# Optimization experiments

Hardware: AMD Instinct MI355X
Metric: run time of the kernel (lower is better)

Reference implementation:

```python
import jax, jax.numpy as jnp
import numpy as np

B, S, D, H = 2, 2048, 1024, 16
DK = D // H  # 64
THETA = 10000.0


def setup_inputs() -> dict:
    key = jax.random.key(0)
    ks = jax.random.split(key, 5)
    sigma = (2.0 / (D + DK)) ** 0.5
    return {
        "x": jax.random.normal(ks[0], (B, S, D), jnp.float32),
        "Wq": jax.random.normal(ks[1], (D, H * DK), jnp.float32) * sigma,
        "Wk": jax.random.normal(ks[2], (D, H * DK), jnp.float32) * sigma,
        "Wv": jax.random.normal(ks[3], (D, H * DK), jnp.float32) * sigma,
        "Wo": jax.random.normal(ks[4], (D, H * DK), jnp.float32) * sigma,
        "token_positions": jnp.arange(S, dtype=jnp.int32),
    }


def _rope(x, pos):
    # x: (B, H, S, DK); pos: (S,). Block-diag 2x2 rotation == paired rotation.
    half = DK // 2
    k = jnp.arange(half, dtype=jnp.float32)
    inv_freq = 1.0 / (THETA ** (2.0 * k / DK))          # (half,)
    ang = pos.astype(jnp.float32)[:, None] * inv_freq    # (S, half)
    cos, sin = jnp.cos(ang), jnp.sin(ang)
    xr = x.reshape(*x.shape[:-1], half, 2)
    x0, x1 = xr[..., 0], xr[..., 1]
    o0 = x0 * cos - x1 * sin
    o1 = x0 * sin + x1 * cos
    return jnp.stack([o0, o1], axis=-1).reshape(x.shape)


def reference(x, Wq, Wk, Wv, Wo, token_positions):
    # projections: einsum('... d_in, hd d_in -> ... hd') == x @ W.T
    def proj(W):
        return (x @ W.T).reshape(B, S, H, DK).transpose(0, 2, 1, 3)  # (B,H,S,DK)

    q, k, v = proj(Wq), proj(Wk), proj(Wv)
    q = _rope(q, token_positions)
    k = _rope(k, token_positions)

    scores = jnp.einsum("bhqd,bhkd->bhqk", q, k) / jnp.sqrt(jnp.float32(DK))
    causal = jnp.tril(jnp.ones((S, S), bool))  # (S,S), True where attended
    scores = jnp.where(causal[None, None], scores, -jnp.inf)
    probs = jax.nn.softmax(scores, axis=-1)

    o = jnp.einsum("bhqk,bhkd->bhqd", probs, v)
    o = o.transpose(0, 2, 1, 3).reshape(B, S, H * DK)
    return o @ Wo.T  # einsum('... d_out, d_model d_out -> ... d_model')
```

## Files before the change

kernel.cpp:

```cpp
#include <hip/hip_runtime.h>

typedef __bf16 bf16;
typedef __bf16 bf16x4 __attribute__((ext_vector_type(4)));
typedef __bf16 bf16x8 __attribute__((ext_vector_type(8)));
typedef float f32x4 __attribute__((ext_vector_type(4)));

#define MFMA16(a, b, c) __builtin_amdgcn_mfma_f32_16x16x32_bf16((a), (b), (c), 0, 0, 0)

constexpr int B_ = 2, S_ = 2048, D_ = 1024, H_ = 16, DK_ = 64;

__device__ __forceinline__ void gload16(const bf16* g, bf16* l)
{
  __builtin_amdgcn_global_load_lds(
      (const __attribute__((address_space(1))) uint32_t*)g,
      (__attribute__((address_space(3))) uint32_t*)l, 16, 0, 0);
}

__global__ __launch_bounds__(256) void cvt_k(
    const float* __restrict__ x, const float* __restrict__ Wq, const float* __restrict__ Wk,
    const float* __restrict__ Wv, const float* __restrict__ Wo, bf16* __restrict__ ws)
{
  size_t f = ((size_t)blockIdx.x * 256 + threadIdx.x) * 4;
  const float* src;
  bf16* dst;
  size_t off;
  if (f < 4194304) {
    src = x; dst = ws; off = f;
  } else {
    size_t g = f - 4194304;
    int wsel = (int)(g >> 20);
    off = g & 1048575;
    src = wsel == 0 ? Wq : wsel == 1 ? Wk : wsel == 2 ? Wv : Wo;
    dst = ws + 4194304 + ((size_t)wsel << 20);
  }
  float4 v = *(const float4*)(src + off);
  bf16x4 o = {(bf16)v.x, (bf16)v.y, (bf16)v.z, (bf16)v.w};
  *(bf16x4*)(dst + off) = o;
}

template <typename TY, int PERM>
__global__ __launch_bounds__(256) void gemm_k(
    const bf16* __restrict__ A,
    const bf16* __restrict__ W0, const bf16* __restrict__ W1, const bf16* __restrict__ W2,
    TY* __restrict__ Y0, TY* __restrict__ Y1, TY* __restrict__ Y2,
    int Kdim, float scale0)
{
  __shared__ __align__(16) bf16 As[128 * 64];
  __shared__ __align__(16) bf16 Bs[128 * 64];
  const int t = threadIdx.x, l = t & 63, w = t >> 6;
  const int wm = w >> 1, wn = w & 1;
  const int m0 = blockIdx.x * 128, n0 = blockIdx.y * 128;
  const int z = blockIdx.z;
  const bf16* W = z == 0 ? W0 : z == 1 ? W1 : W2;
  TY* Y = z == 0 ? Y0 : z == 1 ? Y1 : Y2;
  const float scale = (PERM == 1 && z == 0) ? scale0 : 1.0f;

  f32x4 acc[4][4] = {};

  for (int k0 = 0; k0 < Kdim; k0 += 64) {
    __syncthreads();
#pragma unroll
    for (int j = 0; j < 4; ++j) {
      int slot = j * 256 + t;
      int row = slot >> 3, c8 = slot & 7;
      int csw = (c8 ^ (row & 7)) << 3;
      gload16(A + (size_t)(m0 + row) * Kdim + k0 + csw, &As[(j * 256 + w * 64) * 8]);
      gload16(W + (size_t)(n0 + row) * Kdim + k0 + csw, &Bs[(j * 256 + w * 64) * 8]);
    }
    asm volatile("s_waitcnt vmcnt(0)" ::: "memory");
    __syncthreads();
#pragma unroll
    for (int kk = 0; kk < 2; ++kk) {
      bf16x8 af[4], bfr[4];
#pragma unroll
      for (int i = 0; i < 4; ++i) {
        int Ra = wm * 64 + i * 16 + (l & 15);
        int Rb = wn * 64 + i * 16 + (l & 15);
        int c = kk * 4 + (l >> 4);
        af[i] = *(const bf16x8*)&As[Ra * 64 + ((c ^ (Ra & 7)) << 3)];
        bfr[i] = *(const bf16x8*)&Bs[Rb * 64 + ((c ^ (Rb & 7)) << 3)];
      }
#pragma unroll
      for (int mi = 0; mi < 4; ++mi)
#pragma unroll
        for (int ni = 0; ni < 4; ++ni)
          acc[mi][ni] = MFMA16(af[mi], bfr[ni], acc[mi][ni]);
    }
  }

#pragma unroll
  for (int mi = 0; mi < 4; ++mi)
#pragma unroll
    for (int ni = 0; ni < 4; ++ni)
#pragma unroll
      for (int j = 0; j < 4; ++j) {
        int m = m0 + wm * 64 + mi * 16 + (l >> 4) * 4 + j;
        int n = n0 + wn * 64 + ni * 16 + (l & 15);
        float v = acc[mi][ni][j] * scale;
        if (PERM == 0) {
          Y[(size_t)m * 1024 + n] = (TY)v;
        } else {
          int b = m >> 11, s = m & (S_ - 1), h = n >> 6, d = n & (DK_ - 1);
          Y[(((size_t)(b * H_ + h)) * S_ + s) * DK_ + d] = (TY)v;
        }
      }
}

__global__ __launch_bounds__(256) void rope_k(
    bf16* __restrict__ K, const int* __restrict__ pos)
{
  int idx = blockIdx.x * 256 + threadIdx.x;
  int kpg = idx & 3;
  int s = (idx >> 2) & (S_ - 1);
  int bh = idx >> 13;
  float p = (float)pos[s];
  size_t off = ((size_t)bh * S_ + s) * DK_ + kpg * 16;
  bf16x8 lo = *(const bf16x8*)(K + off);
  bf16x8 hi = *(const bf16x8*)(K + off + 8);
  bf16x8 olo, ohi;
#pragma unroll
  for (int ii = 0; ii < 8; ++ii) {
    int kp = kpg * 8 + ii;
    float ang = p * exp2f((float)kp * -0.41524101186017f);
    float sn, cs;
    __sincosf(ang, &sn, &cs);
    float x0 = (float)((ii < 4 ? lo : hi)[(ii & 3) * 2]);
    float x1 = (float)((ii < 4 ? lo : hi)[(ii & 3) * 2 + 1]);
    bf16 o0 = (bf16)(x0 * cs - x1 * sn);
    bf16 o1 = (bf16)(x0 * sn + x1 * cs);
    if (ii < 4) { olo[(ii & 3) * 2] = o0; olo[(ii & 3) * 2 + 1] = o1; }
    else        { ohi[(ii & 3) * 2] = o0; ohi[(ii & 3) * 2 + 1] = o1; }
  }
  *(bf16x8*)(K + off) = olo;
  *(bf16x8*)(K + off + 8) = ohi;
}

__global__ __launch_bounds__(256, 4) void attn_k(
    const bf16* __restrict__ Q, const bf16* __restrict__ K, const bf16* __restrict__ V,
    const int* __restrict__ pos, bf16* __restrict__ O)
{
  __shared__ __align__(16) bf16 Klds[2][64 * 64];
  __shared__ __align__(16) bf16 Vt[2][64 * 64];
  __shared__ __align__(16) bf16 Ps[4][16 * 64];

  const int t = threadIdx.x, l = t & 63, w = t >> 6;
  const int bx = blockIdx.x;
  const int i5 = bx >> 5;
  const int bh = bx & 31;
  const int a = i5 & 7, bq = i5 >> 3;
  const int qt = (bq == 0) ? (31 - a) : (bq == 1) ? a : (bq == 2) ? (16 + a) : (15 - a);
  const int b = bh >> 4, h = bh & 15;
  const size_t base = (size_t)bh * S_ * DK_;
  const int q0 = qt * 64;

  const int qrow = w * 16 + (l & 15), qcol = (l >> 4) * 8;
  const bf16* pq = Q + base + (size_t)(q0 + qrow) * 64 + qcol;
  bf16x8 aq0 = *(const bf16x8*)pq, aq1 = *(const bf16x8*)(pq + 32);
  {
    float p = (float)pos[q0 + qrow];
#pragma unroll
    for (int i2 = 0; i2 < 4; ++i2) {
      int kp = (l >> 4) * 4 + i2;
      float s0, c0, s1, c1;
      __sincosf(p * exp2f((float)kp * -0.41524101186017f), &s0, &c0);
      __sincosf(p * exp2f((float)(kp + 16) * -0.41524101186017f), &s1, &c1);
      float x0 = (float)aq0[2 * i2], x1 = (float)aq0[2 * i2 + 1];
      aq0[2 * i2] = (bf16)(x0 * c0 - x1 * s0);
      aq0[2 * i2 + 1] = (bf16)(x0 * s0 + x1 * c0);
      x0 = (float)aq1[2 * i2]; x1 = (float)aq1[2 * i2 + 1];
      aq1[2 * i2] = (bf16)(x0 * c1 - x1 * s1);
      aq1[2 * i2 + 1] = (bf16)(x0 * s1 + x1 * c1);
    }
  }

  {
#pragma unroll
    for (int j = 0; j < 2; ++j) {
      int slot = j * 256 + t, row = slot >> 3, c8 = slot & 7;
      gload16(K + base + (size_t)row * 64 + ((c8 ^ (row & 7)) << 3),
              &Klds[0][(j * 256 + w * 64) * 8]);
    }
    const bf16* pv = V + base + (size_t)l * 64 + w * 16;
    bf16x8 v0 = *(const bf16x8*)pv, v1 = *(const bf16x8*)(pv + 8);
    asm volatile("s_waitcnt vmcnt(0)" ::: "memory");
#pragma unroll
    for (int ii = 0; ii < 8; ++ii) {
      int d0 = w * 16 + ii, d1 = w * 16 + 8 + ii;
      Vt[0][d0 * 64 + (((l >> 3) ^ (d0 & 7)) << 3) + (l & 7)] = v0[ii];
      Vt[0][d1 * 64 + (((l >> 3) ^ (d1 & 7)) << 3) + (l & 7)] = v1[ii];
    }
  }
  __syncthreads();

  f32x4 acc[4] = {};
  float lsum[4] = {0.f, 0.f, 0.f, 0.f};

  int cur = 0;
  for (int tk = 0; tk <= qt; ++tk) {
    const int nxt = cur ^ 1;
    const bool hasn = tk < qt;
    bf16x8 v0, v1;
    if (hasn) {
      const int kv0n = (tk + 1) * 64;
#pragma unroll
      for (int j = 0; j < 2; ++j) {
        int slot = j * 256 + t, row = slot >> 3, c8 = slot & 7;
        gload16(K + base + (size_t)(kv0n + row) * 64 + ((c8 ^ (row & 7)) << 3),
                &Klds[nxt][(j * 256 + w * 64) * 8]);
      }
      const bf16* pv = V + base + (size_t)(kv0n + l) * 64 + w * 16;
      v0 = *(const bf16x8*)pv;
      v1 = *(const bf16x8*)(pv + 8);
    }

    f32x4 sc[4];
    __builtin_amdgcn_s_setprio(1);
#pragma unroll
    for (int nf = 0; nf < 4; ++nf) {
      int R = nf * 16 + (l & 15);
      int c0 = l >> 4;
      bf16x8 b0 = *(const bf16x8*)&Klds[cur][R * 64 + ((c0 ^ (R & 7)) << 3)];
      bf16x8 b1 = *(const bf16x8*)&Klds[cur][R * 64 + (((4 + c0) ^ (R & 7)) << 3)];
      f32x4 s = {};
      s = MFMA16(aq0, b0, s);
      s = MFMA16(aq1, b1, s);
      sc[nf] = s;
    }
    __builtin_amdgcn_s_setprio(0);

    if (tk == qt) {
#pragma unroll
      for (int nf = 0; nf < 4; ++nf)
#pragma unroll
        for (int j = 0; j < 4; ++j) {
          int kvl = nf * 16 + (l & 15);
          int ql = w * 16 + (l >> 4) * 4 + j;
          if (kvl > ql) sc[nf][j] = -1e30f;
        }
    }

#pragma unroll
    for (int nf = 0; nf < 4; ++nf)
#pragma unroll
      for (int j = 0; j < 4; ++j) {
        float p = exp2f(sc[nf][j]);
        lsum[j] += p;
        int r = (l >> 4) * 4 + j, c = nf * 16 + (l & 15);
        Ps[w][r * 64 + ((((c >> 3) ^ (r & 7))) << 3) + (c & 7)] = (bf16)p;
      }

    asm volatile("s_waitcnt lgkmcnt(0)" ::: "memory");

    __builtin_amdgcn_s_setprio(1);
#pragma unroll
    for (int kk = 0; kk < 2; ++kk) {
      int rp = l & 15;
      int c8p = kk * 4 + (l >> 4);
      bf16x8 ap = *(const bf16x8*)&Ps[w][rp * 64 + ((c8p ^ (rp & 7)) << 3)];
#pragma unroll
      for (int nf = 0; nf < 4; ++nf) {
        int R = nf * 16 + (l & 15);
        bf16x8 bv = *(const bf16x8*)&Vt[cur][R * 64 + ((c8p ^ (R & 7)) << 3)];
        acc[nf] = MFMA16(ap, bv, acc[nf]);
      }
    }
    __builtin_amdgcn_s_setprio(0);

    if (hasn) {
#pragma unroll
      for (int ii = 0; ii < 8; ++ii) {
        int d0 = w * 16 + ii, d1 = w * 16 + 8 + ii;
        Vt[nxt][d0 * 64 + (((l >> 3) ^ (d0 & 7)) << 3) + (l & 7)] = v0[ii];
        Vt[nxt][d1 * 64 + (((l >> 3) ^ (d1 & 7)) << 3) + (l & 7)] = v1[ii];
      }
      asm volatile("s_waitcnt vmcnt(0)" ::: "memory");
    }
    __syncthreads();
    cur = nxt;
  }

#pragma unroll
  for (int m = 1; m <= 8; m <<= 1)
#pragma unroll
    for (int j = 0; j < 4; ++j)
      lsum[j] += __shfl_xor(lsum[j], m, 64);

#pragma unroll
  for (int nf = 0; nf < 4; ++nf)
#pragma unroll
    for (int j = 0; j < 4; ++j) {
      int r = w * 16 + (l >> 4) * 4 + j;
      int d = nf * 16 + (l & 15);
      O[((size_t)(b * S_ + q0 + r) * H_ + h) * DK_ + d] = (bf16)(acc[nf][j] / lsum[j]);
    }
}

extern "C" void kernel_launch(void* const* d_in, const int* in_sizes, int n_in,
                              void* d_out, int out_size, void* d_ws, size_t ws_size,
                              hipStream_t stream)
{
  const float* x = (const float*)d_in[0];
  const float* Wq = (const float*)d_in[1];
  const float* Wk = (const float*)d_in[2];
  const float* Wv = (const float*)d_in[3];
  const float* Wo = (const float*)d_in[4];
  const int* pos = (const int*)d_in[5];

  bf16* ws = (bf16*)d_ws;
  const size_t NE = (size_t)B_ * H_ * S_ * DK_;
  bf16* xb = ws;
  bf16* Wqb = ws + NE;
  bf16* Wkb = Wqb + 1048576;
  bf16* Wvb = Wkb + 1048576;
  bf16* Wob = Wvb + 1048576;
  bf16* Qb = Wob + 1048576;
  bf16* Kb = Qb + NE;
  bf16* Vb = Kb + NE;
  bf16* Ob = xb;

  dim3 blk(256);

  hipLaunchKernelGGL(cvt_k, dim3(8192), blk, 0, stream, x, Wq, Wk, Wv, Wo, ws);

  hipLaunchKernelGGL((gemm_k<bf16, 1>), dim3(32, 8, 3), blk, 0, stream,
                     xb, Wqb, Wkb, Wvb, Qb, Kb, Vb, 1024, 0.125f * 1.4426950408889634f);

  hipLaunchKernelGGL(rope_k, dim3(1024), blk, 0, stream, Kb, pos);

  hipLaunchKernelGGL(attn_k, dim3(1024), blk, 0, stream, Qb, Kb, Vb, pos, Ob);

  hipLaunchKernelGGL((gemm_k<float, 0>), dim3(32, 8, 1), blk, 0, stream,
                     Ob, Wob, Wob, Wob, (float*)d_out, (float*)d_out, (float*)d_out,
                     1024, 1.0f);
}
```

Baseline: 128.5 us.

## Enlarge attention blocks to 128 query rows with 8 waves sharing KV tiles

The attention kernel now runs 512-thread blocks covering 128 query rows (two 64-row query tiles), so each K/V tile loaded into LDS is reused by twice as many waves. Loads per thread are halved, and waves whose query tile is already finished skip compute on the last KV tile. This cuts global K/V traffic and the number of blocks, but halves the grid to 512 blocks. It also adds idle waves on the diagonal tile and puts more waves behind each barrier.

```diff
diff --git a/kernel.cpp b/kernel.cpp
--- a/kernel.cpp
+++ b/kernel.cpp
@@ -135,23 +135,26 @@
   *(bf16x8*)(K + off + 8) = ohi;
 }
 
-__global__ __launch_bounds__(256, 4) void attn_k(
+__global__ __launch_bounds__(512, 2) void attn_k(
     const bf16* __restrict__ Q, const bf16* __restrict__ K, const bf16* __restrict__ V,
     const int* __restrict__ pos, bf16* __restrict__ O)
 {
   __shared__ __align__(16) bf16 Klds[2][64 * 64];
   __shared__ __align__(16) bf16 Vt[2][64 * 64];
-  __shared__ __align__(16) bf16 Ps[4][16 * 64];
+  __shared__ __align__(16) bf16 Ps[8][16 * 64];
 
   const int t = threadIdx.x, l = t & 63, w = t >> 6;
+  const int wl = w & 3;
   const int bx = blockIdx.x;
   const int i5 = bx >> 5;
   const int bh = bx & 31;
   const int a = i5 & 7, bq = i5 >> 3;
-  const int qt = (bq == 0) ? (31 - a) : (bq == 1) ? a : (bq == 2) ? (16 + a) : (15 - a);
+  const int qt2 = bq ? a : (15 - a);
   const int b = bh >> 4, h = bh & 15;
   const size_t base = (size_t)bh * S_ * DK_;
-  const int q0 = qt * 64;
+  const int q0 = qt2 * 128;
+  const int ntk = 2 * qt2 + 2;
+  const int myqt = 2 * qt2 + (w >> 2);
 
   const int qrow = w * 16 + (l & 15), qcol = (l >> 4) * 8;
   const bf16* pq = Q + base + (size_t)(q0 + qrow) * 64 + qcol;
@@ -174,20 +177,16 @@
   }
 
   {
-#pragma unroll
-    for (int j = 0; j < 2; ++j) {
-      int slot = j * 256 + t, row = slot >> 3, c8 = slot & 7;
-      gload16(K + base + (size_t)row * 64 + ((c8 ^ (row & 7)) << 3),
-              &Klds[0][(j * 256 + w * 64) * 8]);
-    }
-    const bf16* pv = V + base + (size_t)l * 64 + w * 16;
-    bf16x8 v0 = *(const bf16x8*)pv, v1 = *(const bf16x8*)(pv + 8);
+    int row = t >> 3, c8 = t & 7;
+    gload16(K + base + (size_t)row * 64 + ((c8 ^ (row & 7)) << 3),
+            &Klds[0][(w * 64) * 8]);
+    const bf16* pv = V + base + (size_t)l * 64 + w * 8;
+    bf16x8 v0 = *(const bf16x8*)pv;
     asm volatile("s_waitcnt vmcnt(0)" ::: "memory");
 #pragma unroll
     for (int ii = 0; ii < 8; ++ii) {
-      int d0 = w * 16 + ii, d1 = w * 16 + 8 + ii;
+      int d0 = w * 8 + ii;
       Vt[0][d0 * 64 + (((l >> 3) ^ (d0 & 7)) << 3) + (l & 7)] = v0[ii];
-      Vt[0][d1 * 64 + (((l >> 3) ^ (d1 & 7)) << 3) + (l & 7)] = v1[ii];
     }
   }
   __syncthreads();
@@ -196,82 +195,78 @@
   float lsum[4] = {0.f, 0.f, 0.f, 0.f};
 
   int cur = 0;
-  for (int tk = 0; tk <= qt; ++tk) {
+  for (int tk = 0; tk < ntk; ++tk) {
     const int nxt = cur ^ 1;
-    const bool hasn = tk < qt;
-    bf16x8 v0, v1;
+    const bool hasn = (tk + 1) < ntk;
+    bf16x8 v0;
     if (hasn) {
       const int kv0n = (tk + 1) * 64;
-#pragma unroll
-      for (int j = 0; j < 2; ++j) {
-        int slot = j * 256 + t, row = slot >> 3, c8 = slot & 7;
-        gload16(K + base + (size_t)(kv0n + row) * 64 + ((c8 ^ (row & 7)) << 3),
-                &Klds[nxt][(j * 256 + w * 64) * 8]);
-      }
-      const bf16* pv = V + base + (size_t)(kv0n + l) * 64 + w * 16;
-      v0 = *(const bf16x8*)pv;
-      v1 = *(const bf16x8*)(pv + 8);
-    }
-
-    f32x4 sc[4];
-    __builtin_amdgcn_s_setprio(1);
-#pragma unroll
-    for (int nf = 0; nf < 4; ++nf) {
-      int R = nf * 16 + (l & 15);
-      int c0 = l >> 4;
-      bf16x8 b0 = *(const bf16x8*)&Klds[cur][R * 64 + ((c0 ^ (R & 7)) << 3)];
-      bf16x8 b1 = *(const bf16x8*)&Klds[cur][R * 64 + (((4 + c0) ^ (R & 7)) << 3)];
-      f32x4 s = {};
-      s = MFMA16(aq0, b0, s);
-      s = MFMA16(aq1, b1, s);
-      sc[nf] = s;
-    }
-    __builtin_amdgcn_s_setprio(0);
-
-    if (tk == qt) {
-#pragma unroll
-      for (int nf = 0; nf < 4; ++nf)
-#pragma unroll
-        for (int j = 0; j < 4; ++j) {
-          int kvl = nf * 16 + (l & 15);
-          int ql = w * 16 + (l >> 4) * 4 + j;
-          if (kvl > ql) sc[nf][j] = -1e30f;
-        }
-    }
-
-#pragma unroll
-    for (int nf = 0; nf < 4; ++nf)
-#pragma unroll
-      for (int j = 0; j < 4; ++j) {
-        float p = exp2f(sc[nf][j]);
-        lsum[j] += p;
-        int r = (l >> 4) * 4 + j, c = nf * 16 + (l & 15);
-        Ps[w][r * 64 + ((((c >> 3) ^ (r & 7))) << 3) + (c & 7)] = (bf16)p;
-      }
-
-    asm volatile("s_waitcnt lgkmcnt(0)" ::: "memory");
-
-    __builtin_amdgcn_s_setprio(1);
-#pragma unroll
-    for (int kk = 0; kk < 2; ++kk) {
-      int rp = l & 15;
-      int c8p = kk * 4 + (l >> 4);
-      bf16x8 ap = *(const bf16x8*)&Ps[w][rp * 64 + ((c8p ^ (rp & 7)) << 3)];
+      int row = t >> 3, c8 = t & 7;
+      gload16(K + base + (size_t)(kv0n + row) * 64 + ((c8 ^ (row & 7)) << 3),
+              &Klds[nxt][(w * 64) * 8]);
+      v0 = *(const bf16x8*)(V + base + (size_t)(kv0n + l) * 64 + w * 8);
+    }
+
+    if (tk <= myqt) {
+      f32x4 sc[4];
+      __builtin_amdgcn_s_setprio(1);
 #pragma unroll
       for (int nf = 0; nf < 4; ++nf) {
         int R = nf * 16 + (l & 15);
-        bf16x8 bv = *(const bf16x8*)&Vt[cur][R * 64 + ((c8p ^ (R & 7)) << 3)];
-        acc[nf] = MFMA16(ap, bv, acc[nf]);
-      }
-    }
-    __builtin_amdgcn_s_setprio(0);
+        int c0 = l >> 4;
+        bf16x8 b0 = *(const bf16x8*)&Klds[cur][R * 64 + ((c0 ^ (R & 7)) << 3)];
+        bf16x8 b1 = *(const bf16x8*)&Klds[cur][R * 64 + (((4 + c0) ^ (R & 7)) << 3)];
+        f32x4 s = {};
+        s = MFMA16(aq0, b0, s);
+        s = MFMA16(aq1, b1, s);
+        sc[nf] = s;
+      }
+      __builtin_amdgcn_s_setprio(0);
+
+      if (tk == myqt) {
+#pragma unroll
+        for (int nf = 0; nf < 4; ++nf)
+#pragma unroll
+          for (int j = 0; j < 4; ++j) {
+            int kvl = nf * 16 + (l & 15);
+            int ql = wl * 16 + (l >> 4) * 4 + j;
+            if (kvl > ql) sc[nf][j] = -1e30f;
+          }
+      }
+
+#pragma unroll
+      for (int nf = 0; nf < 4; ++nf)
+#pragma unroll
+        for (int j = 0; j < 4; ++j) {
+          float p = exp2f(sc[nf][j]);
+          lsum[j] += p;
+          int r = (l >> 4) * 4 + j, c = nf * 16 + (l & 15);
+          Ps[w][r * 64 + ((((c >> 3) ^ (r & 7))) << 3) + (c & 7)] = (bf16)p;
+        }
+
+      asm volatile("s_waitcnt lgkmcnt(0)" ::: "memory");
+
+      __builtin_amdgcn_s_setprio(1);
+#pragma unroll
+      for (int kk = 0; kk < 2; ++kk) {
+        int rp = l & 15;
+        int c8p = kk * 4 + (l >> 4);
+        bf16x8 ap = *(const bf16x8*)&Ps[w][rp * 64 + ((c8p ^ (rp & 7)) << 3)];
+#pragma unroll
+        for (int nf = 0; nf < 4; ++nf) {
+          int R = nf * 16 + (l & 15);
+          bf16x8 bv = *(const bf16x8*)&Vt[cur][R * 64 + ((c8p ^ (R & 7)) << 3)];
+          acc[nf] = MFMA16(ap, bv, acc[nf]);
+        }
+      }
+      __builtin_amdgcn_s_setprio(0);
+    }
 
     if (hasn) {
 #pragma unroll
       for (int ii = 0; ii < 8; ++ii) {
-        int d0 = w * 16 + ii, d1 = w * 16 + 8 + ii;
+        int d0 = w * 8 + ii;
         Vt[nxt][d0 * 64 + (((l >> 3) ^ (d0 & 7)) << 3) + (l & 7)] = v0[ii];
-        Vt[nxt][d1 * 64 + (((l >> 3) ^ (d1 & 7)) << 3) + (l & 7)] = v1[ii];
       }
       asm volatile("s_waitcnt vmcnt(0)" ::: "memory");
     }
@@ -327,7 +322,7 @@
 
   hipLaunchKernelGGL(rope_k, dim3(1024), blk, 0, stream, Kb, pos);
 
-  hipLaunchKernelGGL(attn_k, dim3(1024), blk, 0, stream, Qb, Kb, Vb, pos, Ob);
+  hipLaunchKernelGGL(attn_k, dim3(512), dim3(512), 0, stream, Qb, Kb, Vb, pos, Ob);
 
   hipLaunchKernelGGL((gemm_k<float, 0>), dim3(32, 8, 1), blk, 0, stream,
                      Ob, Wob, Wob, Wob, (float*)d_out, (float*)d_out, (float*)d_out,
```

Result: no change. 129.6 us (+0.8%).
